# Performance work log

Hardware: AMD Instinct MI355X
Metric: run time of the kernel (lower is better)

The kernel has to match this reference:

```python
import jax, jax.numpy as jnp
import numpy as np

N, E, D, R, L = 50000, 250000, 256, 8, 3


def setup_inputs() -> dict:
    key = jax.random.key(0)
    k = jax.random.split(key, 7)
    scale = 1.0 / np.sqrt(D)
    x = jax.random.normal(k[0], (N, D), dtype=jnp.float32)
    edge_index = jax.random.randint(k[1], (2, E), 0, N, dtype=jnp.int64)
    edge_type = jax.random.randint(k[2], (E,), 0, R, dtype=jnp.int64)
    W_rel = jax.random.normal(k[3], (L, R, D, D), dtype=jnp.float32) * scale
    W_root = jax.random.normal(k[4], (L, D, D), dtype=jnp.float32) * scale
    bias = jax.random.normal(k[5], (L, D), dtype=jnp.float32) * 0.02
    return {"x": x, "edge_index": edge_index, "edge_type": edge_type,
            "W_rel": W_rel, "W_root": W_root, "bias": bias}


def reference(x, edge_index, edge_type, W_rel, W_root, bias):
    # RGCNEncoder on the flattened (offset-concatenated) graph:
    # L layers of: h = relu( x @ W_root + b + scatter_add_dst( W_rel[rt] @ x[src] ) )
    src, dst = edge_index[0], edge_index[1]
    n_layers = W_rel.shape[0]
    for l in range(n_layers):  # small fixed layer loop
        # per-relation transform of ALL nodes, then gather per edge by (relation, src)
        xr = jnp.einsum('nd,rde->rne', x, W_rel[l])        # [R, N, D]
        msg = xr[edge_type, src]                           # [E, D] gather
        agg = jax.ops.segment_sum(msg, dst, num_segments=x.shape[0])  # scatter-add
        x = jax.nn.relu(agg + x @ W_root[l] + bias[l])
    return x
```

## Files before the change

kernel.cpp:

```cpp
#include <hip/hip_runtime.h>

#define NN 50000
#define NE 250000
#define DD 256
#define NREL 8
#define NL 3

#define NSRCB ((NN + 127) / 128)
#define NBKT (NREL * NSRCB)

typedef __attribute__((ext_vector_type(8))) short short8;
typedef __attribute__((ext_vector_type(4))) float floatx4;

#if __has_builtin(__builtin_amdgcn_global_load_lds)
#define GLOAD16(g, l) __builtin_amdgcn_global_load_lds( \
    (__attribute__((address_space(1))) void*)(void*)(g), \
    (__attribute__((address_space(3))) void*)(void*)(l), 16, 0, 0)
#else
#define GLOAD16(g, l) do { *(uint4*)(l) = *(const uint4*)(g); } while (0)
#endif

__device__ inline unsigned short f2bf(float f) {
    unsigned int u = __builtin_bit_cast(unsigned int, f);
    u += 0x7FFFu + ((u >> 16) & 1u);
    return (unsigned short)(u >> 16);
}
__device__ inline float bf2f(unsigned short u) {
    unsigned int x = ((unsigned int)u) << 16;
    return __builtin_bit_cast(float, x);
}

__global__ void zero_ints(int* __restrict__ p, int n) {
    int i = blockIdx.x * blockDim.x + threadIdx.x;
    if (i < n) p[i] = 0;
}

__global__ void hist_bkt(const int* __restrict__ ei, const int* __restrict__ et,
                         int* __restrict__ bktCnt) {
    int e = blockIdx.x * blockDim.x + threadIdx.x;
    if (e < NE) atomicAdd(&bktCnt[et[e] * NSRCB + (ei[e] >> 7)], 1);
}

__global__ __launch_bounds__(256)
void scan_part(const int* __restrict__ cnt, int n, int* __restrict__ blockSums) {
    __shared__ int ps[256];
    const int b = blockIdx.x, t = threadIdx.x;
    const int base = b * 1024 + t * 4;
    int s = 0;
#pragma unroll
    for (int j = 0; j < 4; ++j) s += (base + j < n) ? cnt[base + j] : 0;
    ps[t] = s;
    __syncthreads();
    for (int o = 128; o > 0; o >>= 1) {
        if (t < o) ps[t] += ps[t + o];
        __syncthreads();
    }
    if (t == 0) blockSums[b] = ps[0];
}

__global__ __launch_bounds__(256)
void scan_tops(const int* __restrict__ blockSums, int nb, int* __restrict__ blockOffs) {
    __shared__ int ps[256];
    const int t = threadIdx.x;
    ps[t] = (t < nb) ? blockSums[t] : 0;
    __syncthreads();
    for (int o = 1; o < 256; o <<= 1) {
        int x = (t >= o) ? ps[t - o] : 0;
        __syncthreads();
        ps[t] += x;
        __syncthreads();
    }
    blockOffs[t] = (t == 0) ? 0 : ps[t - 1];
}

__global__ __launch_bounds__(256)
void scan_local(const int* __restrict__ cnt, int n, int total,
                const int* __restrict__ blockOffs,
                int* __restrict__ offs, int* __restrict__ cur) {
    __shared__ int ps[256];
    const int b = blockIdx.x, t = threadIdx.x;
    const int base = b * 1024 + t * 4;
    int v[4];
#pragma unroll
    for (int j = 0; j < 4; ++j) v[j] = (base + j < n) ? cnt[base + j] : 0;
    int s = v[0] + v[1] + v[2] + v[3];
    ps[t] = s;
    __syncthreads();
    for (int o = 1; o < 256; o <<= 1) {
        int x = (t >= o) ? ps[t - o] : 0;
        __syncthreads();
        ps[t] += x;
        __syncthreads();
    }
    int run = blockOffs[b] + ((t == 0) ? 0 : ps[t - 1]);
#pragma unroll
    for (int j = 0; j < 4; ++j) {
        if (base + j < n) { offs[base + j] = run; cur[base + j] = run; run += v[j]; }
    }
    if (b == 0 && t == 0) offs[n] = total;
}

__global__ void mk_reloffs(const int* __restrict__ bktOff, int* __restrict__ relOffs) {
    const int t = threadIdx.x;
    if (t < NREL) relOffs[t] = bktOff[t * NSRCB];
    if (t == 0) relOffs[NREL] = NE;
}

__global__ void scatter_bkt(const int* __restrict__ ei, const int* __restrict__ et,
                            int* __restrict__ bktCur, int* __restrict__ ssrc,
                            int* __restrict__ sdst) {
    int e = blockIdx.x * blockDim.x + threadIdx.x;
    if (e < NE) {
        int s = ei[e];
        int p = atomicAdd(&bktCur[et[e] * NSRCB + (s >> 7)], 1);
        ssrc[p] = s;
        sdst[p] = ei[NE + e];
    }
}

__global__ void hist_dst(const int* __restrict__ sdst, int* __restrict__ dstCnt) {
    int p = blockIdx.x * blockDim.x + threadIdx.x;
    if (p < NE) atomicAdd(&dstCnt[sdst[p]], 1);
}

__global__ void mk_mpos(const int* __restrict__ sdst, int* __restrict__ dstCur,
                        int* __restrict__ mpos) {
    int p = blockIdx.x * blockDim.x + threadIdx.x;
    if (p < NE) mpos[p] = atomicAdd(&dstCur[sdst[p]], 1);
}

__global__ void transpose_bf16(const float* __restrict__ src, unsigned short* __restrict__ dst) {
    __shared__ float t[32][33];
    const size_t mb = (size_t)blockIdx.x * DD * DD;
    const int d0 = blockIdx.y * 32, e0 = blockIdx.z * 32;
    const int tx = threadIdx.x, ty = threadIdx.y;
#pragma unroll
    for (int i = 0; i < 4; ++i)
        t[ty + 8 * i][tx] = src[mb + (size_t)(d0 + ty + 8 * i) * DD + e0 + tx];
    __syncthreads();
#pragma unroll
    for (int i = 0; i < 4; ++i)
        dst[mb + (size_t)(e0 + ty + 8 * i) * DD + d0 + tx] = f2bf(t[tx][ty + 8 * i]);
}

__global__ void conv_bf16(const float4* __restrict__ s, ushort4* __restrict__ d, int n4) {
    int i = blockIdx.x * blockDim.x + threadIdx.x;
    const int stride = gridDim.x * blockDim.x;
    for (; i < n4; i += stride) {
        float4 v = s[i];
        d[i] = make_ushort4(f2bf(v.x), f2bf(v.y), f2bf(v.z), f2bf(v.w));
    }
}

__global__ void relu_convert(float4* __restrict__ p, ushort4* __restrict__ xb, int n4) {
    int i = blockIdx.x * blockDim.x + threadIdx.x;
    const int stride = gridDim.x * blockDim.x;
    for (; i < n4; i += stride) {
        float4 v = p[i];
        v.x = v.x > 0.f ? v.x : 0.f;
        v.y = v.y > 0.f ? v.y : 0.f;
        v.z = v.z > 0.f ? v.z : 0.f;
        v.w = v.w > 0.f ? v.w : 0.f;
        p[i] = v;
        xb[i] = make_ushort4(f2bf(v.x), f2bf(v.y), f2bf(v.z), f2bf(v.w));
    }
}

__global__ __launch_bounds__(256)
void root_gemm_mfma(const unsigned short* __restrict__ Xb, const unsigned short* __restrict__ WT,
                    const float* __restrict__ bias, float* __restrict__ C)
{
    __shared__ unsigned short As[128][32];
    __shared__ unsigned short Bs[128][32];
    const int tid = threadIdx.x;
    const int lane = tid & 63;
    const int w = tid >> 6;
    const int wr = w >> 1, wc = w & 1;
    const int m0 = blockIdx.x * 128;
    const int n0 = blockIdx.y * 128;
    const int srow = tid >> 2;
    const int sq = tid & 3;

    floatx4 acc[4][4] = {};

    for (int kt = 0; kt < DD / 32; ++kt) {
        const int k0 = kt * 32;
        int r0 = min(m0 + srow, NN - 1);
        int r1 = min(m0 + srow + 64, NN - 1);
        GLOAD16(&Xb[(size_t)r0 * DD + k0 + sq * 8], &As[srow][sq * 8]);
        GLOAD16(&Xb[(size_t)r1 * DD + k0 + sq * 8], &As[srow + 64][sq * 8]);
        GLOAD16(&WT[(size_t)(n0 + srow) * DD + k0 + sq * 8], &Bs[srow][sq * 8]);
        GLOAD16(&WT[(size_t)(n0 + srow + 64) * DD + k0 + sq * 8], &Bs[srow + 64][sq * 8]);
        __syncthreads();
        short8 a[4], b[4];
#pragma unroll
        for (int mi = 0; mi < 4; ++mi)
            a[mi] = *(const short8*)&As[wr * 64 + mi * 16 + (lane & 15)][(lane >> 4) * 8];
#pragma unroll
        for (int ni = 0; ni < 4; ++ni)
            b[ni] = *(const short8*)&Bs[wc * 64 + ni * 16 + (lane & 15)][(lane >> 4) * 8];
#pragma unroll
        for (int mi = 0; mi < 4; ++mi)
#pragma unroll
            for (int ni = 0; ni < 4; ++ni)
                acc[mi][ni] = __builtin_amdgcn_mfma_f32_16x16x32_bf16(a[mi], b[ni], acc[mi][ni], 0, 0, 0);
        __syncthreads();
    }

    const int cq = lane >> 4;
    const int cn = lane & 15;
#pragma unroll
    for (int mi = 0; mi < 4; ++mi) {
#pragma unroll
        for (int q = 0; q < 4; ++q) {
            int row = m0 + wr * 64 + mi * 16 + cq * 4 + q;
            if (row < NN) {
#pragma unroll
                for (int ni = 0; ni < 4; ++ni) {
                    int col = n0 + wc * 64 + ni * 16 + cn;
                    C[(size_t)row * DD + col] = acc[mi][ni][q] + bias[col];
                }
            }
        }
    }
}

__global__ __launch_bounds__(256)
void edge_msgs(const unsigned short* __restrict__ Xb, const unsigned short* __restrict__ WTl,
               const int* __restrict__ ssrc, const int* __restrict__ mpos,
               const int* __restrict__ relOffs, unsigned short* __restrict__ msgs,
               int n0base, int MCOLS)
{
    __shared__ unsigned short As[128][32];
    __shared__ unsigned short Bs[128][32];
    __shared__ int srcs[128];
    __shared__ int mposs[128];

    const int t = blockIdx.x;
    int rel = -1, base = 0, cnt = 0, accT = 0;
#pragma unroll
    for (int r = 0; r < NREL; ++r) {
        int s = relOffs[r], e = relOffs[r + 1];
        int nt = (e - s + 127) / 128;
        if (rel < 0 && t < accT + nt) {
            rel = r;
            base = s + (t - accT) * 128;
            cnt = min(128, e - base);
        }
        accT += nt;
    }
    if (rel < 0) return;

    const int tid = threadIdx.x;
    if (tid < 128) {
        int idx = base + tid;
        srcs[tid] = (tid < cnt) ? ssrc[idx] : 0;
        mposs[tid] = (tid < cnt) ? mpos[idx] : 0;
    }
    __syncthreads();

    const unsigned short* WT = WTl + (size_t)rel * DD * DD;

    const int lane = tid & 63;
    const int w = tid >> 6;
    const int wr = w >> 1, wc = w & 1;
    const int n0 = n0base + blockIdx.y * 128;
    const int srow = tid >> 2;
    const int sq = tid & 3;

    floatx4 acc[4][4] = {};

    for (int kt = 0; kt < DD / 32; ++kt) {
        const int k0 = kt * 32;
        int r0 = srcs[srow];
        int r1 = srcs[srow + 64];
        GLOAD16(&Xb[(size_t)r0 * DD + k0 + sq * 8], &As[srow][sq * 8]);
        GLOAD16(&Xb[(size_t)r1 * DD + k0 + sq * 8], &As[srow + 64][sq * 8]);
        GLOAD16(&WT[(size_t)(n0 + srow) * DD + k0 + sq * 8], &Bs[srow][sq * 8]);
        GLOAD16(&WT[(size_t)(n0 + srow + 64) * DD + k0 + sq * 8], &Bs[srow + 64][sq * 8]);
        __syncthreads();
        short8 a[4], b[4];
#pragma unroll
        for (int mi = 0; mi < 4; ++mi)
            a[mi] = *(const short8*)&As[wr * 64 + mi * 16 + (lane & 15)][(lane >> 4) * 8];
#pragma unroll
        for (int ni = 0; ni < 4; ++ni)
            b[ni] = *(const short8*)&Bs[wc * 64 + ni * 16 + (lane & 15)][(lane >> 4) * 8];
#pragma unroll
        for (int mi = 0; mi < 4; ++mi)
#pragma unroll
            for (int ni = 0; ni < 4; ++ni)
                acc[mi][ni] = __builtin_amdgcn_mfma_f32_16x16x32_bf16(a[mi], b[ni], acc[mi][ni], 0, 0, 0);
        __syncthreads();
    }

    const int cq = lane >> 4;
    const int cn = lane & 15;
#pragma unroll
    for (int mi = 0; mi < 4; ++mi) {
#pragma unroll
        for (int q = 0; q < 4; ++q) {
            int slot = wr * 64 + mi * 16 + cq * 4 + q;
            if (slot < cnt) {
                size_t mrow = (size_t)mposs[slot] * MCOLS + blockIdx.y * 128 + wc * 64;
#pragma unroll
                for (int ni = 0; ni < 4; ++ni)
                    msgs[mrow + ni * 16 + cn] = f2bf(acc[mi][ni][q]);
            }
        }
    }
}

__global__ __launch_bounds__(256)
void combine4(const unsigned short* __restrict__ msgs, const int* __restrict__ dstOffs,
              float* __restrict__ out, unsigned short* __restrict__ xb)
{
    int v = blockIdx.x * 4 + (threadIdx.x >> 6);
    if (v >= NN) return;
    const int lane = threadIdx.x & 63;
    const size_t rb = (size_t)v * DD + lane * 4;
    float4 a = *(const float4*)&out[rb];
    const int b0 = dstOffs[v], b1 = dstOffs[v + 1];
    for (int k = b0; k < b1; ++k) {
        ushort4 m = *(const ushort4*)&msgs[(size_t)k * DD + lane * 4];
        a.x += bf2f(m.x); a.y += bf2f(m.y); a.z += bf2f(m.z); a.w += bf2f(m.w);
    }
    a.x = a.x > 0.f ? a.x : 0.f;
    a.y = a.y > 0.f ? a.y : 0.f;
    a.z = a.z > 0.f ? a.z : 0.f;
    a.w = a.w > 0.f ? a.w : 0.f;
    *(float4*)&out[rb] = a;
    *(ushort4*)&xb[rb] = make_ushort4(f2bf(a.x), f2bf(a.y), f2bf(a.z), f2bf(a.w));
}

__global__ __launch_bounds__(256)
void combine2(const unsigned short* __restrict__ msgs, const int* __restrict__ dstOffs,
              float* __restrict__ out, int colbase)
{
    int v = blockIdx.x * 4 + (threadIdx.x >> 6);
    if (v >= NN) return;
    const int lane = threadIdx.x & 63;
    const size_t rb = (size_t)v * DD + colbase + lane * 2;
    float2 a = *(const float2*)&out[rb];
    const int b0 = dstOffs[v], b1 = dstOffs[v + 1];
    for (int k = b0; k < b1; ++k) {
        ushort2 m = *(const ushort2*)&msgs[(size_t)k * 128 + lane * 2];
        a.x += bf2f(m.x); a.y += bf2f(m.y);
    }
    a.x = a.x > 0.f ? a.x : 0.f;
    a.y = a.y > 0.f ? a.y : 0.f;
    *(float2*)&out[rb] = a;
}

__global__ __launch_bounds__(256)
void edge_gemm_mfma(const unsigned short* __restrict__ Xb, const unsigned short* __restrict__ WTl,
                    const int* __restrict__ ssrc, const int* __restrict__ sdst,
                    const int* __restrict__ offsets, float* __restrict__ out)
{
    __shared__ unsigned short As[128][32];
    __shared__ unsigned short Bs[128][32];
    __shared__ int srcs[128];
    __shared__ int dsts[128];

    const int t = blockIdx.x;
    int rel = -1, base = 0, cnt = 0, accT = 0;
#pragma unroll
    for (int r = 0; r < NREL; ++r) {
        int s = offsets[r], e = offsets[r + 1];
        int nt = (e - s + 127) / 128;
        if (rel < 0 && t < accT + nt) {
            rel = r;
            base = s + (t - accT) * 128;
            cnt = min(128, e - base);
        }
        accT += nt;
    }
    if (rel < 0) return;

    const int tid = threadIdx.x;
    if (tid < 128) {
        int idx = base + tid;
        srcs[tid] = (tid < cnt) ? ssrc[idx] : 0;
        dsts[tid] = (tid < cnt) ? sdst[idx] : 0;
    }
    __syncthreads();

    const unsigned short* WT = WTl + (size_t)rel * DD * DD;
    const int lane = tid & 63;
    const int w = tid >> 6;
    const int wr = w >> 1, wc = w & 1;
    const int n0 = blockIdx.y * 128;
    const int srow = tid >> 2;
    const int sq = tid & 3;

    floatx4 acc[4][4] = {};

    for (int kt = 0; kt < DD / 32; ++kt) {
        const int k0 = kt * 32;
        int r0 = srcs[srow];
        int r1 = srcs[srow + 64];
        GLOAD16(&Xb[(size_t)r0 * DD + k0 + sq * 8], &As[srow][sq * 8]);
        GLOAD16(&Xb[(size_t)r1 * DD + k0 + sq * 8], &As[srow + 64][sq * 8]);
        GLOAD16(&WT[(size_t)(n0 + srow) * DD + k0 + sq * 8], &Bs[srow][sq * 8]);
        GLOAD16(&WT[(size_t)(n0 + srow + 64) * DD + k0 + sq * 8], &Bs[srow + 64][sq * 8]);
        __syncthreads();
        short8 a[4], b[4];
#pragma unroll
        for (int mi = 0; mi < 4; ++mi)
            a[mi] = *(const short8*)&As[wr * 64 + mi * 16 + (lane & 15)][(lane >> 4) * 8];
#pragma unroll
        for (int ni = 0; ni < 4; ++ni)
            b[ni] = *(const short8*)&Bs[wc * 64 + ni * 16 + (lane & 15)][(lane >> 4) * 8];
#pragma unroll
        for (int mi = 0; mi < 4; ++mi)
#pragma unroll
            for (int ni = 0; ni < 4; ++ni)
                acc[mi][ni] = __builtin_amdgcn_mfma_f32_16x16x32_bf16(a[mi], b[ni], acc[mi][ni], 0, 0, 0);
        __syncthreads();
    }

    const int cq = lane >> 4;
    const int cn = lane & 15;
#pragma unroll
    for (int mi = 0; mi < 4; ++mi) {
#pragma unroll
        for (int q = 0; q < 4; ++q) {
            int slot = wr * 64 + mi * 16 + cq * 4 + q;
            if (slot < cnt) {
                int d = dsts[slot];
#pragma unroll
                for (int ni = 0; ni < 4; ++ni) {
                    int col = n0 + wc * 64 + ni * 16 + cn;
                    atomicAdd(&out[(size_t)d * DD + col], acc[mi][ni][q]);
                }
            }
        }
    }
}

extern "C" void kernel_launch(void* const* d_in, const int* in_sizes, int n_in,
                              void* d_out, int out_size, void* d_ws, size_t ws_size,
                              hipStream_t stream)
{
    const float* x      = (const float*)d_in[0];
    const int*   ei     = (const int*)d_in[1];
    const int*   et     = (const int*)d_in[2];
    const float* W_rel  = (const float*)d_in[3];
    const float* W_root = (const float*)d_in[4];
    const float* bias   = (const float*)d_in[5];
    float* out = (float*)d_out;

    unsigned char* wsb = (unsigned char*)d_ws;
    size_t off = 0;
    auto alloc = [&](size_t bytes) -> void* {
        void* p = wsb + off;
        off = (off + bytes + 255) & ~(size_t)255;
        return p;
    };
    unsigned short* xb      = (unsigned short*)alloc((size_t)NN * DD * 2);
    unsigned short* wrelT   = (unsigned short*)alloc((size_t)NL * NREL * DD * DD * 2);
    unsigned short* wrootT  = (unsigned short*)alloc((size_t)NL * DD * DD * 2);
    int* ssrc    = (int*)alloc((size_t)NE * 4);
    int* sdst    = (int*)alloc((size_t)NE * 4);
    int* mpos    = (int*)alloc((size_t)NE * 4);
    int* dstOffs = (int*)alloc((size_t)(NN + 1) * 4);
    int* dstCnt  = (int*)alloc((size_t)NN * 4);
    int* dstCur  = (int*)alloc((size_t)NN * 4);
    int* bktCnt  = (int*)alloc((size_t)NBKT * 4);
    int* bktOff  = (int*)alloc((size_t)(NBKT + 1) * 4);
    int* bktCur  = (int*)alloc((size_t)NBKT * 4);
    int* relOffs = (int*)alloc((size_t)(NREL + 1) * 4);
    int* bktSums = (int*)alloc(256 * 4);
    int* bktBOff = (int*)alloc(256 * 4);
    int* dstSums = (int*)alloc(256 * 4);
    int* dstBOff = (int*)alloc(256 * 4);
    unsigned short* msgs = (unsigned short*)(wsb + off);
    const size_t cap = (ws_size > off) ? ws_size - off : 0;
    const size_t needFull = (size_t)NE * DD * 2;
    const int mode = (cap >= needFull) ? 1 : (cap >= needFull / 2) ? 2 : 0;

    const int nbBkt = (NBKT + 1023) / 1024;
    const int nbDst = (NN + 1023) / 1024;

    transpose_bf16<<<dim3(NL * NREL, DD / 32, DD / 32), dim3(32, 8), 0, stream>>>(W_rel, wrelT);
    transpose_bf16<<<dim3(NL, DD / 32, DD / 32), dim3(32, 8), 0, stream>>>(W_root, wrootT);
    conv_bf16<<<2048, 256, 0, stream>>>((const float4*)x, (ushort4*)xb, NN * DD / 4);

    zero_ints<<<(NBKT + 255) / 256, 256, 0, stream>>>(bktCnt, NBKT);
    hist_bkt<<<(NE + 255) / 256, 256, 0, stream>>>(ei, et, bktCnt);
    scan_part<<<nbBkt, 256, 0, stream>>>(bktCnt, NBKT, bktSums);
    scan_tops<<<1, 256, 0, stream>>>(bktSums, nbBkt, bktBOff);
    scan_local<<<nbBkt, 256, 0, stream>>>(bktCnt, NBKT, NE, bktBOff, bktOff, bktCur);
    mk_reloffs<<<1, 64, 0, stream>>>(bktOff, relOffs);
    scatter_bkt<<<(NE + 255) / 256, 256, 0, stream>>>(ei, et, bktCur, ssrc, sdst);

    if (mode != 0) {
        zero_ints<<<(NN + 255) / 256, 256, 0, stream>>>(dstCnt, NN);
        hist_dst<<<(NE + 255) / 256, 256, 0, stream>>>(sdst, dstCnt);
        scan_part<<<nbDst, 256, 0, stream>>>(dstCnt, NN, dstSums);
        scan_tops<<<1, 256, 0, stream>>>(dstSums, nbDst, dstBOff);
        scan_local<<<nbDst, 256, 0, stream>>>(dstCnt, NN, NE, dstBOff, dstOffs, dstCur);
        mk_mpos<<<(NE + 255) / 256, 256, 0, stream>>>(sdst, dstCur, mpos);
    }

    const int ntiles = (NE + 127) / 128 + NREL;
    const int ncomb = (NN + 3) / 4;

    for (int l = 0; l < NL; ++l) {
        root_gemm_mfma<<<dim3((NN + 127) / 128, DD / 128), 256, 0, stream>>>(
            xb, wrootT + (size_t)l * DD * DD, bias + (size_t)l * DD, out);
        const unsigned short* wl = wrelT + (size_t)l * NREL * DD * DD;
        if (mode == 1) {
            edge_msgs<<<dim3(ntiles, 2), 256, 0, stream>>>(
                xb, wl, ssrc, mpos, relOffs, msgs, 0, DD);
            combine4<<<ncomb, 256, 0, stream>>>(msgs, dstOffs, out, xb);
        } else if (mode == 2) {
            for (int h = 0; h < 2; ++h) {
                edge_msgs<<<dim3(ntiles, 1), 256, 0, stream>>>(
                    xb, wl, ssrc, mpos, relOffs, msgs, h * 128, 128);
                combine2<<<ncomb, 256, 0, stream>>>(msgs, dstOffs, out, h * 128);
            }
            conv_bf16<<<2048, 256, 0, stream>>>((const float4*)out, (ushort4*)xb, NN * DD / 4);
        } else {
            edge_gemm_mfma<<<dim3(ntiles, DD / 128), 256, 0, stream>>>(
                xb, wl, ssrc, sdst, relOffs, out);
            relu_convert<<<2048, 256, 0, stream>>>((float4*)out, (ushort4*)xb, NN * DD / 4);
        }
    }
}
```

Baseline: 491.3 us.

## Write edge messages contiguously, gather via eidx in combine, bf16 root output

Edge messages are now written contiguously in bucket order and the combine step gathers them through an edge-index permutation, replacing the scattered writes to destination-sorted positions. When workspace allows, the root GEMM writes a bf16 buffer, which the combine reads instead of fp32. The combine writes fp32 output only on the last layer and bf16 activations otherwise. The LDS tile layout is reorganised to be k-major, and nontemporal loads and stores are used. The half-width mode 2 path is removed. The trade-off is random gather reads during combine and an extra bf16 rounding of the root term.

```diff
diff --git a/kernel.cpp b/kernel.cpp
--- a/kernel.cpp
+++ b/kernel.cpp
@@ -11,6 +11,8 @@
 
 typedef __attribute__((ext_vector_type(8))) short short8;
 typedef __attribute__((ext_vector_type(4))) float floatx4;
+typedef __attribute__((ext_vector_type(2))) unsigned int u32x2;
+typedef __attribute__((ext_vector_type(4))) float f32x4v;
 
 #if __has_builtin(__builtin_amdgcn_global_load_lds)
 #define GLOAD16(g, l) __builtin_amdgcn_global_load_lds( \
@@ -123,10 +125,13 @@
     if (p < NE) atomicAdd(&dstCnt[sdst[p]], 1);
 }
 
-__global__ void mk_mpos(const int* __restrict__ sdst, int* __restrict__ dstCur,
-                        int* __restrict__ mpos) {
+__global__ void mk_eidx(const int* __restrict__ sdst, int* __restrict__ dstCur,
+                        int* __restrict__ eidx) {
     int p = blockIdx.x * blockDim.x + threadIdx.x;
-    if (p < NE) mpos[p] = atomicAdd(&dstCur[sdst[p]], 1);
+    if (p < NE) {
+        int q = atomicAdd(&dstCur[sdst[p]], 1);
+        eidx[q] = p;
+    }
 }
 
 __global__ void transpose_bf16(const float* __restrict__ src, unsigned short* __restrict__ dst) {
@@ -167,38 +172,43 @@
 }
 
 __global__ __launch_bounds__(256)
-void root_gemm_mfma(const unsigned short* __restrict__ Xb, const unsigned short* __restrict__ WT,
-                    const float* __restrict__ bias, float* __restrict__ C)
+void root_gemm_k(const unsigned short* __restrict__ Xb, const unsigned short* __restrict__ WT,
+                 const float* __restrict__ bias, float* __restrict__ Cf,
+                 unsigned short* __restrict__ Cb, int useB)
 {
-    __shared__ unsigned short As[128][32];
-    __shared__ unsigned short Bs[128][32];
+    __shared__ unsigned short AsF[512 * 8];
+    __shared__ unsigned short BsF[512 * 8];
     const int tid = threadIdx.x;
     const int lane = tid & 63;
     const int w = tid >> 6;
     const int wr = w >> 1, wc = w & 1;
     const int m0 = blockIdx.x * 128;
     const int n0 = blockIdx.y * 128;
-    const int srow = tid >> 2;
-    const int sq = tid & 3;
+
+    const int s1 = tid, s2 = tid + 256;
+    const int k16a = s1 >> 7, ra = s1 & 127;
+    const int k16b = s2 >> 7, rb2 = s2 & 127;
+    const int ar0 = min(m0 + ra, NN - 1);
+    const int ar1 = min(m0 + rb2, NN - 1);
 
     floatx4 acc[4][4] = {};
 
     for (int kt = 0; kt < DD / 32; ++kt) {
         const int k0 = kt * 32;
-        int r0 = min(m0 + srow, NN - 1);
-        int r1 = min(m0 + srow + 64, NN - 1);
-        GLOAD16(&Xb[(size_t)r0 * DD + k0 + sq * 8], &As[srow][sq * 8]);
-        GLOAD16(&Xb[(size_t)r1 * DD + k0 + sq * 8], &As[srow + 64][sq * 8]);
-        GLOAD16(&WT[(size_t)(n0 + srow) * DD + k0 + sq * 8], &Bs[srow][sq * 8]);
-        GLOAD16(&WT[(size_t)(n0 + srow + 64) * DD + k0 + sq * 8], &Bs[srow + 64][sq * 8]);
-        __syncthreads();
+        GLOAD16(&Xb[(size_t)ar0 * DD + k0 + k16a * 8], &AsF[s1 * 8]);
+        GLOAD16(&Xb[(size_t)ar1 * DD + k0 + k16b * 8], &AsF[s2 * 8]);
+        GLOAD16(&WT[(size_t)(n0 + ra) * DD + k0 + k16a * 8], &BsF[s1 * 8]);
+        GLOAD16(&WT[(size_t)(n0 + rb2) * DD + k0 + k16b * 8], &BsF[s2 * 8]);
+        __syncthreads();
+        const int k16 = lane >> 4;
+        const int fr = lane & 15;
         short8 a[4], b[4];
 #pragma unroll
         for (int mi = 0; mi < 4; ++mi)
-            a[mi] = *(const short8*)&As[wr * 64 + mi * 16 + (lane & 15)][(lane >> 4) * 8];
+            a[mi] = *(const short8*)&AsF[(k16 * 128 + wr * 64 + mi * 16 + fr) * 8];
 #pragma unroll
         for (int ni = 0; ni < 4; ++ni)
-            b[ni] = *(const short8*)&Bs[wc * 64 + ni * 16 + (lane & 15)][(lane >> 4) * 8];
+            b[ni] = *(const short8*)&BsF[(k16 * 128 + wc * 64 + ni * 16 + fr) * 8];
 #pragma unroll
         for (int mi = 0; mi < 4; ++mi)
 #pragma unroll
@@ -218,7 +228,11 @@
 #pragma unroll
                 for (int ni = 0; ni < 4; ++ni) {
                     int col = n0 + wc * 64 + ni * 16 + cn;
-                    C[(size_t)row * DD + col] = acc[mi][ni][q] + bias[col];
+                    float val = acc[mi][ni][q] + bias[col];
+                    if (useB)
+                        __builtin_nontemporal_store(f2bf(val), &Cb[(size_t)row * DD + col]);
+                    else
+                        Cf[(size_t)row * DD + col] = val;
                 }
             }
         }
@@ -226,15 +240,13 @@
 }
 
 __global__ __launch_bounds__(256)
-void edge_msgs(const unsigned short* __restrict__ Xb, const unsigned short* __restrict__ WTl,
-               const int* __restrict__ ssrc, const int* __restrict__ mpos,
-               const int* __restrict__ relOffs, unsigned short* __restrict__ msgs,
-               int n0base, int MCOLS)
+void edge_msgs_c(const unsigned short* __restrict__ Xb, const unsigned short* __restrict__ WTl,
+                 const int* __restrict__ ssrc, const int* __restrict__ relOffs,
+                 unsigned short* __restrict__ msgs)
 {
-    __shared__ unsigned short As[128][32];
-    __shared__ unsigned short Bs[128][32];
+    __shared__ unsigned short AsF[512 * 8];
+    __shared__ unsigned short BsF[512 * 8];
     __shared__ int srcs[128];
-    __shared__ int mposs[128];
 
     const int t = blockIdx.x;
     int rel = -1, base = 0, cnt = 0, accT = 0;
@@ -255,7 +267,6 @@
     if (tid < 128) {
         int idx = base + tid;
         srcs[tid] = (tid < cnt) ? ssrc[idx] : 0;
-        mposs[tid] = (tid < cnt) ? mpos[idx] : 0;
     }
     __syncthreads();
 
@@ -264,28 +275,29 @@
     const int lane = tid & 63;
     const int w = tid >> 6;
     const int wr = w >> 1, wc = w & 1;
-    const int n0 = n0base + blockIdx.y * 128;
-    const int srow = tid >> 2;
-    const int sq = tid & 3;
+    const int n0 = blockIdx.y * 128;
+    const int s1 = tid, s2 = tid + 256;
+    const int k16a = s1 >> 7, ra = s1 & 127;
+    const int k16b = s2 >> 7, rb2 = s2 & 127;
 
     floatx4 acc[4][4] = {};
 
     for (int kt = 0; kt < DD / 32; ++kt) {
         const int k0 = kt * 32;
-        int r0 = srcs[srow];
-        int r1 = srcs[srow + 64];
-        GLOAD16(&Xb[(size_t)r0 * DD + k0 + sq * 8], &As[srow][sq * 8]);
-        GLOAD16(&Xb[(size_t)r1 * DD + k0 + sq * 8], &As[srow + 64][sq * 8]);
-        GLOAD16(&WT[(size_t)(n0 + srow) * DD + k0 + sq * 8], &Bs[srow][sq * 8]);
-        GLOAD16(&WT[(size_t)(n0 + srow + 64) * DD + k0 + sq * 8], &Bs[srow + 64][sq * 8]);
-        __syncthreads();
+        GLOAD16(&Xb[(size_t)srcs[ra] * DD + k0 + k16a * 8], &AsF[s1 * 8]);
+        GLOAD16(&Xb[(size_t)srcs[rb2] * DD + k0 + k16b * 8], &AsF[s2 * 8]);
+        GLOAD16(&WT[(size_t)(n0 + ra) * DD + k0 + k16a * 8], &BsF[s1 * 8]);
+        GLOAD16(&WT[(size_t)(n0 + rb2) * DD + k0 + k16b * 8], &BsF[s2 * 8]);
+        __syncthreads();
+        const int k16 = lane >> 4;
+        const int fr = lane & 15;
         short8 a[4], b[4];
 #pragma unroll
         for (int mi = 0; mi < 4; ++mi)
-            a[mi] = *(const short8*)&As[wr * 64 + mi * 16 + (lane & 15)][(lane >> 4) * 8];
+            a[mi] = *(const short8*)&AsF[(k16 * 128 + wr * 64 + mi * 16 + fr) * 8];
 #pragma unroll
         for (int ni = 0; ni < 4; ++ni)
-            b[ni] = *(const short8*)&Bs[wc * 64 + ni * 16 + (lane & 15)][(lane >> 4) * 8];
+            b[ni] = *(const short8*)&BsF[(k16 * 128 + wc * 64 + ni * 16 + fr) * 8];
 #pragma unroll
         for (int mi = 0; mi < 4; ++mi)
 #pragma unroll
@@ -302,54 +314,54 @@
         for (int q = 0; q < 4; ++q) {
             int slot = wr * 64 + mi * 16 + cq * 4 + q;
             if (slot < cnt) {
-                size_t mrow = (size_t)mposs[slot] * MCOLS + blockIdx.y * 128 + wc * 64;
+                size_t mrow = (size_t)(base + slot) * DD + blockIdx.y * 128 + wc * 64;
 #pragma unroll
                 for (int ni = 0; ni < 4; ++ni)
-                    msgs[mrow + ni * 16 + cn] = f2bf(acc[mi][ni][q]);
+                    __builtin_nontemporal_store(f2bf(acc[mi][ni][q]), &msgs[mrow + ni * 16 + cn]);
             }
         }
     }
 }
 
 __global__ __launch_bounds__(256)
-void combine4(const unsigned short* __restrict__ msgs, const int* __restrict__ dstOffs,
-              float* __restrict__ out, unsigned short* __restrict__ xb)
+void combine_g(const unsigned short* __restrict__ msgs, const int* __restrict__ dstOffs,
+               const int* __restrict__ eidx, const unsigned short* __restrict__ rootb,
+               const float* __restrict__ rootf, float* __restrict__ out,
+               unsigned short* __restrict__ xb, int useRootB, int last)
 {
     int v = blockIdx.x * 4 + (threadIdx.x >> 6);
     if (v >= NN) return;
     const int lane = threadIdx.x & 63;
     const size_t rb = (size_t)v * DD + lane * 4;
-    float4 a = *(const float4*)&out[rb];
+    float4 a;
+    if (useRootB) {
+        u32x2 r = __builtin_nontemporal_load((const u32x2*)&rootb[rb]);
+        a.x = bf2f((unsigned short)(r.x & 0xffff));
+        a.y = bf2f((unsigned short)(r.x >> 16));
+        a.z = bf2f((unsigned short)(r.y & 0xffff));
+        a.w = bf2f((unsigned short)(r.y >> 16));
+    } else {
+        a = *(const float4*)&rootf[rb];
+    }
     const int b0 = dstOffs[v], b1 = dstOffs[v + 1];
-    for (int k = b0; k < b1; ++k) {
-        ushort4 m = *(const ushort4*)&msgs[(size_t)k * DD + lane * 4];
-        a.x += bf2f(m.x); a.y += bf2f(m.y); a.z += bf2f(m.z); a.w += bf2f(m.w);
+    for (int q = b0; q < b1; ++q) {
+        int p = eidx[q];
+        u32x2 m = __builtin_nontemporal_load((const u32x2*)&msgs[(size_t)p * DD + lane * 4]);
+        a.x += bf2f((unsigned short)(m.x & 0xffff));
+        a.y += bf2f((unsigned short)(m.x >> 16));
+        a.z += bf2f((unsigned short)(m.y & 0xffff));
+        a.w += bf2f((unsigned short)(m.y >> 16));
     }
     a.x = a.x > 0.f ? a.x : 0.f;
     a.y = a.y > 0.f ? a.y : 0.f;
     a.z = a.z > 0.f ? a.z : 0.f;
     a.w = a.w > 0.f ? a.w : 0.f;
-    *(float4*)&out[rb] = a;
-    *(ushort4*)&xb[rb] = make_ushort4(f2bf(a.x), f2bf(a.y), f2bf(a.z), f2bf(a.w));
-}
-
-__global__ __launch_bounds__(256)
-void combine2(const unsigned short* __restrict__ msgs, const int* __restrict__ dstOffs,
-              float* __restrict__ out, int colbase)
-{
-    int v = blockIdx.x * 4 + (threadIdx.x >> 6);
-    if (v >= NN) return;
-    const int lane = threadIdx.x & 63;
-    const size_t rb = (size_t)v * DD + colbase + lane * 2;
-    float2 a = *(const float2*)&out[rb];
-    const int b0 = dstOffs[v], b1 = dstOffs[v + 1];
-    for (int k = b0; k < b1; ++k) {
-        ushort2 m = *(const ushort2*)&msgs[(size_t)k * 128 + lane * 2];
-        a.x += bf2f(m.x); a.y += bf2f(m.y);
-    }
-    a.x = a.x > 0.f ? a.x : 0.f;
-    a.y = a.y > 0.f ? a.y : 0.f;
-    *(float2*)&out[rb] = a;
+    if (last) {
+        f32x4v o = {a.x, a.y, a.z, a.w};
+        __builtin_nontemporal_store(o, (f32x4v*)&out[rb]);
+    } else {
+        *(ushort4*)&xb[rb] = make_ushort4(f2bf(a.x), f2bf(a.y), f2bf(a.z), f2bf(a.w));
+    }
 }
 
 __global__ __launch_bounds__(256)
@@ -462,7 +474,7 @@
     unsigned short* wrootT  = (unsigned short*)alloc((size_t)NL * DD * DD * 2);
     int* ssrc    = (int*)alloc((size_t)NE * 4);
     int* sdst    = (int*)alloc((size_t)NE * 4);
-    int* mpos    = (int*)alloc((size_t)NE * 4);
+    int* eidx    = (int*)alloc((size_t)NE * 4);
     int* dstOffs = (int*)alloc((size_t)(NN + 1) * 4);
     int* dstCnt  = (int*)alloc((size_t)NN * 4);
     int* dstCur  = (int*)alloc((size_t)NN * 4);
@@ -474,10 +486,24 @@
     int* bktBOff = (int*)alloc(256 * 4);
     int* dstSums = (int*)alloc(256 * 4);
     int* dstBOff = (int*)alloc(256 * 4);
-    unsigned short* msgs = (unsigned short*)(wsb + off);
+
     const size_t cap = (ws_size > off) ? ws_size - off : 0;
-    const size_t needFull = (size_t)NE * DD * 2;
-    const int mode = (cap >= needFull) ? 1 : (cap >= needFull / 2) ? 2 : 0;
+    const size_t needMsgs = (size_t)NE * DD * 2;
+    const size_t needRoot = (size_t)NN * DD * 2;
+    int mode;
+    int useRootB;
+    unsigned short* rootb = nullptr;
+    unsigned short* msgs = nullptr;
+    if (cap >= needMsgs + needRoot + 512) {
+        mode = 1; useRootB = 1;
+        rootb = (unsigned short*)alloc(needRoot);
+        msgs  = (unsigned short*)alloc(needMsgs);
+    } else if (cap >= needMsgs) {
+        mode = 1; useRootB = 0;
+        msgs  = (unsigned short*)alloc(needMsgs);
+    } else {
+        mode = 0; useRootB = 0;
+    }
 
     const int nbBkt = (NBKT + 1023) / 1024;
     const int nbDst = (NN + 1023) / 1024;
@@ -494,34 +520,29 @@
     mk_reloffs<<<1, 64, 0, stream>>>(bktOff, relOffs);
     scatter_bkt<<<(NE + 255) / 256, 256, 0, stream>>>(ei, et, bktCur, ssrc, sdst);
 
-    if (mode != 0) {
+    if (mode == 1) {
         zero_ints<<<(NN + 255) / 256, 256, 0, stream>>>(dstCnt, NN);
         hist_dst<<<(NE + 255) / 256, 256, 0, stream>>>(sdst, dstCnt);
         scan_part<<<nbDst, 256, 0, stream>>>(dstCnt, NN, dstSums);
         scan_tops<<<1, 256, 0, stream>>>(dstSums, nbDst, dstBOff);
         scan_local<<<nbDst, 256, 0, stream>>>(dstCnt, NN, NE, dstBOff, dstOffs, dstCur);
-        mk_mpos<<<(NE + 255) / 256, 256, 0, stream>>>(sdst, dstCur, mpos);
+        mk_eidx<<<(NE + 255) / 256, 256, 0, stream>>>(sdst, dstCur, eidx);
     }
 
     const int ntiles = (NE + 127) / 128 + NREL;
     const int ncomb = (NN + 3) / 4;
 
     for (int l = 0; l < NL; ++l) {
-        root_gemm_mfma<<<dim3((NN + 127) / 128, DD / 128), 256, 0, stream>>>(
-            xb, wrootT + (size_t)l * DD * DD, bias + (size_t)l * DD, out);
         const unsigned short* wl = wrelT + (size_t)l * NREL * DD * DD;
         if (mode == 1) {
-            edge_msgs<<<dim3(ntiles, 2), 256, 0, stream>>>(
-                xb, wl, ssrc, mpos, relOffs, msgs, 0, DD);
-            combine4<<<ncomb, 256, 0, stream>>>(msgs, dstOffs, out, xb);
-        } else if (mode == 2) {
-            for (int h = 0; h < 2; ++h) {
-                edge_msgs<<<dim3(ntiles, 1), 256, 0, stream>>>(
-                    xb, wl, ssrc, mpos, relOffs, msgs, h * 128, 128);
-                combine2<<<ncomb, 256, 0, stream>>>(msgs, dstOffs, out, h * 128);
-            }
-            conv_bf16<<<2048, 256, 0, stream>>>((const float4*)out, (ushort4*)xb, NN * DD / 4);
+            root_gemm_k<<<dim3((NN + 127) / 128, DD / 128), 256, 0, stream>>>(
+                xb, wrootT + (size_t)l * DD * DD, bias + (size_t)l * DD, out, rootb, useRootB);
+            edge_msgs_c<<<dim3(ntiles, 2), 256, 0, stream>>>(xb, wl, ssrc, relOffs, msgs);
+            combine_g<<<ncomb, 256, 0, stream>>>(msgs, dstOffs, eidx, rootb, out, out, xb,
+                                                 useRootB, (l == NL - 1) ? 1 : 0);
         } else {
+            root_gemm_k<<<dim3((NN + 127) / 128, DD / 128), 256, 0, stream>>>(
+                xb, wrootT + (size_t)l * DD * DD, bias + (size_t)l * DD, out, nullptr, 0);
             edge_gemm_mfma<<<dim3(ntiles, DD / 128), 256, 0, stream>>>(
                 xb, wl, ssrc, sdst, relOffs, out);
             relu_convert<<<2048, 256, 0, stream>>>((float4*)out, (ushort4*)xb, NN * DD / 4);
```

Result: slower. 695.4 us (+41.5%).
